# Optimization experiments

Hardware: AMD Instinct MI355X
Metric: run time of the kernel (lower is better)

Reference implementation:

```python
import jax, jax.numpy as jnp
import numpy as np


def _layernorm(x, g, b, eps=1e-5):
    mu = x.mean(-1, keepdims=True)
    var = ((x - mu) ** 2).mean(-1, keepdims=True)
    return (x - mu) / jnp.sqrt(var + eps) * g + b


def _bilinear_sample(feat, coords):
    # feat: (B,C,H,W,D); coords: (B,C,N,2) normalized to [-1,1]
    # torch.grid_sample(mode='bilinear', padding_mode='zeros', align_corners=True)
    B, C, H, W, D = feat.shape
    x = (coords[..., 0] + 1.0) * 0.5 * (W - 1)  # grid x -> width axis
    y = (coords[..., 1] + 1.0) * 0.5 * (H - 1)  # grid y -> height axis
    x0 = jnp.floor(x)
    y0 = jnp.floor(y)
    wx1 = x - x0
    wy1 = y - y0
    bi = jnp.arange(B)[:, None, None]
    ci = jnp.arange(C)[None, :, None]

    def corner(yi, xi, w):
        inb = (xi >= 0) & (xi < W) & (yi >= 0) & (yi < H)
        xc = jnp.clip(xi, 0, W - 1).astype(jnp.int32)
        yc = jnp.clip(yi, 0, H - 1).astype(jnp.int32)
        v = feat[bi, ci, yc, xc]  # (B,C,N,D) gather
        return v * (w * inb)[..., None]

    return (corner(y0, x0, (1 - wy1) * (1 - wx1))
            + corner(y0, x0 + 1, (1 - wy1) * wx1)
            + corner(y0 + 1, x0, wy1 * (1 - wx1))
            + corner(y0 + 1, x0 + 1, wy1 * wx1))


def setup_inputs() -> dict:
    key = jax.random.key(0)
    ks = jax.random.split(key, 12)
    B, C, N, D, H, W = 2, 8, 16384, 256, 64, 64
    s = 1.0 / np.sqrt(D).astype(np.float32)
    return {
        "queries": jax.random.normal(ks[0], (B, N, D), jnp.float32),
        "image_features": jax.random.normal(ks[1], (B, C, H, W, D), jnp.float32),
        "pixel_coords": jax.random.uniform(ks[2], (B, C, N, 2), jnp.float32) * 2.0 - 1.0,
        "valid_mask": jax.random.randint(ks[3], (B, C, N), 0, 2).astype(jnp.int32),
        "Wq": jax.random.normal(ks[4], (D, D), jnp.float32) * s,
        "bq": jnp.zeros((D,), jnp.float32),
        "Wkv": jax.random.normal(ks[5], (D, 2 * D), jnp.float32) * s,
        "bkv": jnp.zeros((2 * D,), jnp.float32),
        "Wo": jax.random.normal(ks[6], (D, D), jnp.float32) * s,
        "bo": jnp.zeros((D,), jnp.float32),
        "gamma": jnp.ones((D,), jnp.float32),
        "beta": jnp.zeros((D,), jnp.float32),
    }


def reference(queries, image_features, pixel_coords, valid_mask,
              Wq, bq, Wkv, bkv, Wo, bo, gamma, beta):
    B, N, D = queries.shape
    residual = queries
    qn = _layernorm(queries, gamma, beta)
    sampled = _bilinear_sample(image_features, pixel_coords)      # (B,C,N,D)
    sampled = jnp.transpose(sampled, (0, 2, 1, 3))                 # (B,N,C,D)
    q = qn @ Wq + bq                                               # (B,N,D)
    kv = sampled @ Wkv + bkv                                       # (B,N,C,2D)
    k, v = kv[..., :D], kv[..., D:]
    scores = jnp.einsum('bnd,bncd->bnc', q, k) / jnp.sqrt(jnp.float32(D))
    valid = jnp.transpose(valid_mask, (0, 2, 1)) != 0              # (B,N,C)
    scores = jnp.where(valid, scores, -jnp.inf)
    attn = jax.nn.softmax(scores, axis=-1)
    attn = jnp.where(jnp.isnan(attn), 0.0, attn)                   # all-invalid -> 0
    out = jnp.einsum('bnc,bncd->bnd', attn, v)
    return residual + out @ Wo + bo
```

## Files before the change

kernel.cpp:

```cpp
#include <hip/hip_runtime.h>
#include <math.h>

#define NROWS 32768

typedef __attribute__((ext_vector_type(8))) short short8;
typedef __attribute__((ext_vector_type(4))) float f32x4;

#define WS_ABF    0
#define WS_WVOBF  32768
#define WS_PB     65536
#define WS_BVO    65792
#define WS_SUMA   66048
#define WS_P      98816
#define WS_FEATBF 8487424

__device__ __forceinline__ unsigned short f2bf(float f) {
    unsigned u = __builtin_bit_cast(unsigned, f);
    u += 0x7FFFu + ((u >> 16) & 1u);
    return (unsigned short)(u >> 16);
}
__device__ __forceinline__ float bf_lo(unsigned u) {
    return __builtin_bit_cast(float, u << 16);
}
__device__ __forceinline__ float bf_hi(unsigned u) {
    return __builtin_bit_cast(float, u & 0xFFFF0000u);
}

__global__ __launch_bounds__(256)
void precompute_kernel(const float* __restrict__ Wq, const float* __restrict__ bq,
                       const float* __restrict__ Wkv, const float* __restrict__ bkv,
                       const float* __restrict__ Wo, const float* __restrict__ feat,
                       float* __restrict__ ws) {
    int t = threadIdx.x;
    int blk = blockIdx.x;
    if (blk >= 514) {
        long i = (long)(blk - 514) * 1024 + t * 4;
        float4 v = *(const float4*)(feat + i);
        unsigned lo = (unsigned)f2bf(v.x) | ((unsigned)f2bf(v.y) << 16);
        unsigned hi = (unsigned)f2bf(v.z) | ((unsigned)f2bf(v.w) << 16);
        *(uint2*)((unsigned short*)(ws + WS_FEATBF) + i) = make_uint2(lo, hi);
        return;
    }
    if (blk < 256) {
        int f = blk;
        const float4* wq4 = (const float4*)(Wq + f * 256);
        const float4* wk4 = (const float4*)(Wkv + (long)t * 512);
        float acc = 0.f;
        #pragma unroll 8
        for (int d4 = 0; d4 < 64; ++d4) {
            float4 a = wq4[d4], b = wk4[d4];
            acc += a.x * b.x + a.y * b.y + a.z * b.z + a.w * b.w;
        }
        ((unsigned short*)(ws + WS_ABF))[t * 256 + f] = f2bf(acc);
    } else if (blk < 512) {
        int e = blk - 256;
        float acc = 0.f;
        for (int g = 0; g < 256; ++g)
            acc = fmaf(Wkv[(long)e * 512 + 256 + g], Wo[g * 256 + t], acc);
        ((unsigned short*)(ws + WS_WVOBF))[t * 256 + e] = f2bf(acc);
    } else if (blk == 512) {
        float acc = 0.f;
        for (int d = 0; d < 256; ++d)
            acc = fmaf(bq[d], Wkv[(long)t * 512 + d], acc);
        ws[WS_PB + t] = acc;
    } else {
        float acc = 0.f;
        for (int g = 0; g < 256; ++g)
            acc = fmaf(bkv[256 + g], Wo[g * 256 + t], acc);
        ws[WS_BVO + t] = acc;
    }
}

__global__ __launch_bounds__(256)
void ln_p_mfma(const float* __restrict__ queries, const float* __restrict__ gamma,
               const float* __restrict__ beta, float* __restrict__ ws) {
    __shared__ unsigned short qs[64][264];
    const unsigned short* Abf = (const unsigned short*)(ws + WS_ABF);
    const float* pb = ws + WS_PB;
    float* pbuf = ws + WS_P;
    int tid = threadIdx.x, wave = tid >> 6, lane = tid & 63;
    long row0 = (long)blockIdx.x * 64;

    float4 g4 = *(const float4*)(gamma + 4 * lane);
    float4 b4 = *(const float4*)(beta + 4 * lane);
    for (int rr = 0; rr < 16; ++rr) {
        int r = wave * 16 + rr;
        float4 v = *(const float4*)(queries + (row0 + r) * 256 + 4 * lane);
        float s = v.x + v.y + v.z + v.w;
        s += __shfl_xor(s, 32); s += __shfl_xor(s, 16); s += __shfl_xor(s, 8);
        s += __shfl_xor(s, 4);  s += __shfl_xor(s, 2);  s += __shfl_xor(s, 1);
        float mu = s * 0.00390625f;
        float dx = v.x - mu, dy = v.y - mu, dz = v.z - mu, dw = v.w - mu;
        float vv = dx * dx + dy * dy + dz * dz + dw * dw;
        vv += __shfl_xor(vv, 32); vv += __shfl_xor(vv, 16); vv += __shfl_xor(vv, 8);
        vv += __shfl_xor(vv, 4);  vv += __shfl_xor(vv, 2);  vv += __shfl_xor(vv, 1);
        float rstd = rsqrtf(vv * 0.00390625f + 1e-5f);
        float qx = dx * rstd * g4.x + b4.x;
        float qy = dy * rstd * g4.y + b4.y;
        float qz = dz * rstd * g4.z + b4.z;
        float qw = dw * rstd * g4.w + b4.w;
        unsigned lo = (unsigned)f2bf(qx) | ((unsigned)f2bf(qy) << 16);
        unsigned hi = (unsigned)f2bf(qz) | ((unsigned)f2bf(qw) << 16);
        *(uint2*)&qs[r][4 * lane] = make_uint2(lo, hi);
    }
    __syncthreads();

    int r16 = lane & 15, g = lane >> 4;
    f32x4 zero = {0.f, 0.f, 0.f, 0.f};
    f32x4 acc[4][4];
    #pragma unroll
    for (int mt = 0; mt < 4; ++mt)
        #pragma unroll
        for (int nt = 0; nt < 4; ++nt) acc[mt][nt] = zero;

    #pragma unroll
    for (int ks = 0; ks < 8; ++ks) {
        short8 bfr[4], afr[4];
        #pragma unroll
        for (int nt = 0; nt < 4; ++nt)
            bfr[nt] = *(const short8*)(Abf + ((wave * 64 + nt * 16 + r16) << 8) + ks * 32 + g * 8);
        #pragma unroll
        for (int mt = 0; mt < 4; ++mt)
            afr[mt] = *(const short8*)(&qs[mt * 16 + r16][ks * 32 + g * 8]);
        #pragma unroll
        for (int mt = 0; mt < 4; ++mt)
            #pragma unroll
            for (int nt = 0; nt < 4; ++nt)
                acc[mt][nt] = __builtin_amdgcn_mfma_f32_16x16x32_bf16(afr[mt], bfr[nt], acc[mt][nt], 0, 0, 0);
    }

    float pbv[4];
    #pragma unroll
    for (int nt = 0; nt < 4; ++nt) pbv[nt] = pb[wave * 64 + nt * 16 + r16];
    #pragma unroll
    for (int mt = 0; mt < 4; ++mt)
        #pragma unroll
        for (int nt = 0; nt < 4; ++nt)
            #pragma unroll
            for (int rg = 0; rg < 4; ++rg)
                pbuf[(row0 + mt * 16 + g * 4 + rg) * 256 + wave * 64 + nt * 16 + r16] =
                    acc[mt][nt][rg] + pbv[nt];
}

__global__ __launch_bounds__(256)
void sample_attn_bf(const float* __restrict__ coords, const int* __restrict__ vmask,
                    float* __restrict__ ws) {
    float* pbuf = ws + WS_P;
    float* suma = ws + WS_SUMA;
    const unsigned short* featbf = (const unsigned short*)(ws + WS_FEATBF);
    int tid = threadIdx.x, wave = tid >> 6, lane = tid & 63;
    long row = (long)blockIdx.x * 4 + wave;
    int b = (int)(row >> 14);
    int n = (int)(row & 16383);

    float4 p4 = *(const float4*)(pbuf + row * 256 + 4 * lane);

    float4 sc[8];
    float score[8];
    bool vld[8];
    #pragma unroll
    for (int c = 0; c < 8; ++c) {
        long cb = (long)(b * 8 + c) * 16384 + n;
        float cx = coords[2 * cb];
        float cy = coords[2 * cb + 1];
        vld[c] = (vmask[cb] != 0);
        float x = (cx + 1.f) * 31.5f;
        float y = (cy + 1.f) * 31.5f;
        float x0f = floorf(x), y0f = floorf(y);
        float wx = x - x0f, wy = y - y0f;
        int ix0 = (int)x0f, iy0 = (int)y0f;
        int ix1 = ix0 + 1, iy1 = iy0 + 1;
        float bx0 = (ix0 >= 0 && ix0 < 64) ? 1.f : 0.f;
        float bx1 = (ix1 >= 0 && ix1 < 64) ? 1.f : 0.f;
        float by0 = (iy0 >= 0 && iy0 < 64) ? 1.f : 0.f;
        float by1 = (iy1 >= 0 && iy1 < 64) ? 1.f : 0.f;
        int cx0 = min(max(ix0, 0), 63), cx1 = min(max(ix1, 0), 63);
        int cy0 = min(max(iy0, 0), 63), cy1 = min(max(iy1, 0), 63);
        const unsigned short* fb = featbf + ((long)(b * 8 + c) << 20);
        const uint2* r00 = (const uint2*)(fb + ((cy0 * 64 + cx0) << 8)) + lane;
        const uint2* r01 = (const uint2*)(fb + ((cy0 * 64 + cx1) << 8)) + lane;
        const uint2* r10 = (const uint2*)(fb + ((cy1 * 64 + cx0) << 8)) + lane;
        const uint2* r11 = (const uint2*)(fb + ((cy1 * 64 + cx1) << 8)) + lane;
        float w00 = (1.f - wy) * (1.f - wx) * by0 * bx0;
        float w01 = (1.f - wy) * wx * by0 * bx1;
        float w10 = wy * (1.f - wx) * by1 * bx0;
        float w11 = wy * wx * by1 * bx1;
        uint2 v00 = *r00, v01 = *r01, v10 = *r10, v11 = *r11;
        float4 s;
        s.x = w00 * bf_lo(v00.x) + w01 * bf_lo(v01.x) + w10 * bf_lo(v10.x) + w11 * bf_lo(v11.x);
        s.y = w00 * bf_hi(v00.x) + w01 * bf_hi(v01.x) + w10 * bf_hi(v10.x) + w11 * bf_hi(v11.x);
        s.z = w00 * bf_lo(v00.y) + w01 * bf_lo(v01.y) + w10 * bf_lo(v10.y) + w11 * bf_lo(v11.y);
        s.w = w00 * bf_hi(v00.y) + w01 * bf_hi(v01.y) + w10 * bf_hi(v10.y) + w11 * bf_hi(v11.y);
        sc[c] = s;
        float t = s.x * p4.x + s.y * p4.y + s.z * p4.z + s.w * p4.w;
        t += __shfl_xor(t, 32); t += __shfl_xor(t, 16); t += __shfl_xor(t, 8);
        t += __shfl_xor(t, 4);  t += __shfl_xor(t, 2);  t += __shfl_xor(t, 1);
        score[c] = t * 0.0625f;
    }

    float m = -INFINITY;
    #pragma unroll
    for (int c = 0; c < 8; ++c) if (vld[c]) m = fmaxf(m, score[c]);
    float4 sb = {0.f, 0.f, 0.f, 0.f};
    float sa = 0.f;
    if (m > -INFINITY) {
        float w[8], s = 0.f;
        #pragma unroll
        for (int c = 0; c < 8; ++c) { w[c] = vld[c] ? expf(score[c] - m) : 0.f; s += w[c]; }
        float inv = 1.f / s;
        #pragma unroll
        for (int c = 0; c < 8; ++c) {
            float a = w[c] * inv;
            sb.x = fmaf(a, sc[c].x, sb.x);
            sb.y = fmaf(a, sc[c].y, sb.y);
            sb.z = fmaf(a, sc[c].z, sb.z);
            sb.w = fmaf(a, sc[c].w, sb.w);
        }
        sa = 1.f;
    }
    unsigned lo = (unsigned)f2bf(sb.x) | ((unsigned)f2bf(sb.y) << 16);
    unsigned hi = (unsigned)f2bf(sb.z) | ((unsigned)f2bf(sb.w) << 16);
    ((uint2*)((char*)pbuf + row * 1024))[lane] = make_uint2(lo, hi);
    if (lane == 0) suma[row] = sa;
}

__global__ __launch_bounds__(256)
void final_mfma(const float* __restrict__ queries, const float* __restrict__ bo,
                const float* __restrict__ ws, float* __restrict__ out) {
    __shared__ unsigned short qs[64][264];
    __shared__ float ssu[64];
    const unsigned short* Wvobf = (const unsigned short*)(ws + WS_WVOBF);
    const float* bvo = ws + WS_BVO;
    const float* suma = ws + WS_SUMA;
    const float* pbuf = ws + WS_P;
    int tid = threadIdx.x, wave = tid >> 6, lane = tid & 63;
    long row0 = (long)blockIdx.x * 64;

    for (int rr = 0; rr < 16; ++rr) {
        int r = wave * 16 + rr;
        uint2 v = ((const uint2*)((const char*)pbuf + (row0 + r) * 1024))[lane];
        *(uint2*)&qs[r][4 * lane] = v;
    }
    if (tid < 64) ssu[tid] = suma[row0 + tid];
    __syncthreads();

    int r16 = lane & 15, g = lane >> 4;
    f32x4 zero = {0.f, 0.f, 0.f, 0.f};
    f32x4 acc[4][4];
    #pragma unroll
    for (int mt = 0; mt < 4; ++mt)
        #pragma unroll
        for (int nt = 0; nt < 4; ++nt) acc[mt][nt] = zero;

    #pragma unroll
    for (int ks = 0; ks < 8; ++ks) {
        short8 bfr[4], afr[4];
        #pragma unroll
        for (int nt = 0; nt < 4; ++nt)
            bfr[nt] = *(const short8*)(Wvobf + ((wave * 64 + nt * 16 + r16) << 8) + ks * 32 + g * 8);
        #pragma unroll
        for (int mt = 0; mt < 4; ++mt)
            afr[mt] = *(const short8*)(&qs[mt * 16 + r16][ks * 32 + g * 8]);
        #pragma unroll
        for (int mt = 0; mt < 4; ++mt)
            #pragma unroll
            for (int nt = 0; nt < 4; ++nt)
                acc[mt][nt] = __builtin_amdgcn_mfma_f32_16x16x32_bf16(afr[mt], bfr[nt], acc[mt][nt], 0, 0, 0);
    }

    float bvov[4], bov[4];
    #pragma unroll
    for (int nt = 0; nt < 4; ++nt) {
        int col = wave * 64 + nt * 16 + r16;
        bvov[nt] = bvo[col];
        bov[nt] = bo[col];
    }
    #pragma unroll
    for (int mt = 0; mt < 4; ++mt)
        #pragma unroll
        for (int nt = 0; nt < 4; ++nt)
            #pragma unroll
            for (int rg = 0; rg < 4; ++rg) {
                long row = row0 + mt * 16 + g * 4 + rg;
                int col = wave * 64 + nt * 16 + r16;
                out[row * 256 + col] = queries[row * 256 + col] + acc[mt][nt][rg]
                                     + ssu[mt * 16 + g * 4 + rg] * bvov[nt] + bov[nt];
            }
}

extern "C" void kernel_launch(void* const* d_in, const int* in_sizes, int n_in,
                              void* d_out, int out_size, void* d_ws, size_t ws_size,
                              hipStream_t stream) {
    const float* queries = (const float*)d_in[0];
    const float* feat    = (const float*)d_in[1];
    const float* coords  = (const float*)d_in[2];
    const int*   vmask   = (const int*)  d_in[3];
    const float* Wq      = (const float*)d_in[4];
    const float* bq      = (const float*)d_in[5];
    const float* Wkv     = (const float*)d_in[6];
    const float* bkv     = (const float*)d_in[7];
    const float* Wo      = (const float*)d_in[8];
    const float* bo      = (const float*)d_in[9];
    const float* gamma   = (const float*)d_in[10];
    const float* beta    = (const float*)d_in[11];
    float* out = (float*)d_out;
    float* ws  = (float*)d_ws;

    precompute_kernel<<<514 + 16384, 256, 0, stream>>>(Wq, bq, Wkv, bkv, Wo, feat, ws);
    ln_p_mfma<<<NROWS / 64, 256, 0, stream>>>(queries, gamma, beta, ws);
    sample_attn_bf<<<NROWS / 4, 256, 0, stream>>>(coords, vmask, ws);
    final_mfma<<<NROWS / 64, 256, 0, stream>>>(queries, bo, ws, out);
}
```

Before: 280.2 us.

## Fuse layernorm projection, sampling attention and output GEMM into one row-pipelined kernel

Replaces the three row kernels (LN+P GEMM, sampling/attention, output GEMM) with one kernel that handles 32 rows per block. The intermediate P vectors, attention outputs and per-row sums stay in shared memory instead of going through global workspace. This removes the global write and reread of the fp32 P buffer and the bf16 attention buffer, plus two launch boundaries. The epilogue now writes coalesced float4 stores, and expf becomes __expf. The trade-off is fewer rows per block for MFMA reuse, extra block barriers, and the gather phase sharing a block with the GEMM phases, which may limit latency hiding.

```diff
diff --git a/kernel.cpp b/kernel.cpp
--- a/kernel.cpp
+++ b/kernel.cpp
@@ -10,8 +10,6 @@
 #define WS_WVOBF  32768
 #define WS_PB     65536
 #define WS_BVO    65792
-#define WS_SUMA   66048
-#define WS_P      98816
 #define WS_FEATBF 8487424
 
 __device__ __forceinline__ unsigned short f2bf(float f) {
@@ -71,221 +69,223 @@
     }
 }
 
-__global__ __launch_bounds__(256)
-void ln_p_mfma(const float* __restrict__ queries, const float* __restrict__ gamma,
-               const float* __restrict__ beta, float* __restrict__ ws) {
-    __shared__ unsigned short qs[64][264];
-    const unsigned short* Abf = (const unsigned short*)(ws + WS_ABF);
-    const float* pb = ws + WS_PB;
-    float* pbuf = ws + WS_P;
+#define RPB  32
+#define SLOT 260
+
+__global__ __launch_bounds__(256, 4)
+void fused_rowpipe(const float* __restrict__ queries, const float* __restrict__ gamma,
+                   const float* __restrict__ beta, const float* __restrict__ coords,
+                   const int* __restrict__ vmask, const float* __restrict__ bo,
+                   const float* __restrict__ ws, float* __restrict__ out) {
+    __shared__ float buf[RPB * SLOT + RPB];
+    float* ssu = buf + RPB * SLOT;
+
+    const unsigned short* Abf    = (const unsigned short*)(ws + WS_ABF);
+    const unsigned short* Wvobf  = (const unsigned short*)(ws + WS_WVOBF);
+    const float*          pb     = ws + WS_PB;
+    const float*          bvo    = ws + WS_BVO;
+    const unsigned short* featbf = (const unsigned short*)(ws + WS_FEATBF);
+
     int tid = threadIdx.x, wave = tid >> 6, lane = tid & 63;
-    long row0 = (long)blockIdx.x * 64;
-
-    float4 g4 = *(const float4*)(gamma + 4 * lane);
-    float4 b4 = *(const float4*)(beta + 4 * lane);
-    for (int rr = 0; rr < 16; ++rr) {
-        int r = wave * 16 + rr;
-        float4 v = *(const float4*)(queries + (row0 + r) * 256 + 4 * lane);
-        float s = v.x + v.y + v.z + v.w;
-        s += __shfl_xor(s, 32); s += __shfl_xor(s, 16); s += __shfl_xor(s, 8);
-        s += __shfl_xor(s, 4);  s += __shfl_xor(s, 2);  s += __shfl_xor(s, 1);
-        float mu = s * 0.00390625f;
-        float dx = v.x - mu, dy = v.y - mu, dz = v.z - mu, dw = v.w - mu;
-        float vv = dx * dx + dy * dy + dz * dz + dw * dw;
-        vv += __shfl_xor(vv, 32); vv += __shfl_xor(vv, 16); vv += __shfl_xor(vv, 8);
-        vv += __shfl_xor(vv, 4);  vv += __shfl_xor(vv, 2);  vv += __shfl_xor(vv, 1);
-        float rstd = rsqrtf(vv * 0.00390625f + 1e-5f);
-        float qx = dx * rstd * g4.x + b4.x;
-        float qy = dy * rstd * g4.y + b4.y;
-        float qz = dz * rstd * g4.z + b4.z;
-        float qw = dw * rstd * g4.w + b4.w;
-        unsigned lo = (unsigned)f2bf(qx) | ((unsigned)f2bf(qy) << 16);
-        unsigned hi = (unsigned)f2bf(qz) | ((unsigned)f2bf(qw) << 16);
-        *(uint2*)&qs[r][4 * lane] = make_uint2(lo, hi);
+    long row0 = (long)blockIdx.x * RPB;
+
+    {
+        float4 g4 = *(const float4*)(gamma + 4 * lane);
+        float4 b4 = *(const float4*)(beta + 4 * lane);
+        #pragma unroll
+        for (int rr = 0; rr < 8; ++rr) {
+            int r = wave * 8 + rr;
+            float4 v = *(const float4*)(queries + (row0 + r) * 256 + 4 * lane);
+            float s = v.x + v.y + v.z + v.w;
+            s += __shfl_xor(s, 32); s += __shfl_xor(s, 16); s += __shfl_xor(s, 8);
+            s += __shfl_xor(s, 4);  s += __shfl_xor(s, 2);  s += __shfl_xor(s, 1);
+            float mu = s * 0.00390625f;
+            float dx = v.x - mu, dy = v.y - mu, dz = v.z - mu, dw = v.w - mu;
+            float vv = dx * dx + dy * dy + dz * dz + dw * dw;
+            vv += __shfl_xor(vv, 32); vv += __shfl_xor(vv, 16); vv += __shfl_xor(vv, 8);
+            vv += __shfl_xor(vv, 4);  vv += __shfl_xor(vv, 2);  vv += __shfl_xor(vv, 1);
+            float rstd = rsqrtf(vv * 0.00390625f + 1e-5f);
+            float qx = dx * rstd * g4.x + b4.x;
+            float qy = dy * rstd * g4.y + b4.y;
+            float qz = dz * rstd * g4.z + b4.z;
+            float qw = dw * rstd * g4.w + b4.w;
+            unsigned lo = (unsigned)f2bf(qx) | ((unsigned)f2bf(qy) << 16);
+            unsigned hi = (unsigned)f2bf(qz) | ((unsigned)f2bf(qw) << 16);
+            *(uint2*)((unsigned short*)&buf[r * SLOT] + 4 * lane) = make_uint2(lo, hi);
+        }
     }
     __syncthreads();
 
     int r16 = lane & 15, g = lane >> 4;
     f32x4 zero = {0.f, 0.f, 0.f, 0.f};
-    f32x4 acc[4][4];
-    #pragma unroll
-    for (int mt = 0; mt < 4; ++mt)
-        #pragma unroll
-        for (int nt = 0; nt < 4; ++nt) acc[mt][nt] = zero;
-
-    #pragma unroll
-    for (int ks = 0; ks < 8; ++ks) {
-        short8 bfr[4], afr[4];
-        #pragma unroll
-        for (int nt = 0; nt < 4; ++nt)
-            bfr[nt] = *(const short8*)(Abf + ((wave * 64 + nt * 16 + r16) << 8) + ks * 32 + g * 8);
-        #pragma unroll
-        for (int mt = 0; mt < 4; ++mt)
-            afr[mt] = *(const short8*)(&qs[mt * 16 + r16][ks * 32 + g * 8]);
-        #pragma unroll
-        for (int mt = 0; mt < 4; ++mt)
+
+    {
+        f32x4 acc[2][4];
+        #pragma unroll
+        for (int mt = 0; mt < 2; ++mt)
+            #pragma unroll
+            for (int nt = 0; nt < 4; ++nt) acc[mt][nt] = zero;
+
+        #pragma unroll
+        for (int ks = 0; ks < 8; ++ks) {
+            short8 bfr[4], afr[2];
             #pragma unroll
             for (int nt = 0; nt < 4; ++nt)
-                acc[mt][nt] = __builtin_amdgcn_mfma_f32_16x16x32_bf16(afr[mt], bfr[nt], acc[mt][nt], 0, 0, 0);
-    }
-
-    float pbv[4];
-    #pragma unroll
-    for (int nt = 0; nt < 4; ++nt) pbv[nt] = pb[wave * 64 + nt * 16 + r16];
-    #pragma unroll
-    for (int mt = 0; mt < 4; ++mt)
-        #pragma unroll
-        for (int nt = 0; nt < 4; ++nt)
-            #pragma unroll
-            for (int rg = 0; rg < 4; ++rg)
-                pbuf[(row0 + mt * 16 + g * 4 + rg) * 256 + wave * 64 + nt * 16 + r16] =
-                    acc[mt][nt][rg] + pbv[nt];
-}
-
-__global__ __launch_bounds__(256)
-void sample_attn_bf(const float* __restrict__ coords, const int* __restrict__ vmask,
-                    float* __restrict__ ws) {
-    float* pbuf = ws + WS_P;
-    float* suma = ws + WS_SUMA;
-    const unsigned short* featbf = (const unsigned short*)(ws + WS_FEATBF);
-    int tid = threadIdx.x, wave = tid >> 6, lane = tid & 63;
-    long row = (long)blockIdx.x * 4 + wave;
-    int b = (int)(row >> 14);
-    int n = (int)(row & 16383);
-
-    float4 p4 = *(const float4*)(pbuf + row * 256 + 4 * lane);
-
-    float4 sc[8];
-    float score[8];
-    bool vld[8];
-    #pragma unroll
-    for (int c = 0; c < 8; ++c) {
-        long cb = (long)(b * 8 + c) * 16384 + n;
-        float cx = coords[2 * cb];
-        float cy = coords[2 * cb + 1];
-        vld[c] = (vmask[cb] != 0);
-        float x = (cx + 1.f) * 31.5f;
-        float y = (cy + 1.f) * 31.5f;
-        float x0f = floorf(x), y0f = floorf(y);
-        float wx = x - x0f, wy = y - y0f;
-        int ix0 = (int)x0f, iy0 = (int)y0f;
-        int ix1 = ix0 + 1, iy1 = iy0 + 1;
-        float bx0 = (ix0 >= 0 && ix0 < 64) ? 1.f : 0.f;
-        float bx1 = (ix1 >= 0 && ix1 < 64) ? 1.f : 0.f;
-        float by0 = (iy0 >= 0 && iy0 < 64) ? 1.f : 0.f;
-        float by1 = (iy1 >= 0 && iy1 < 64) ? 1.f : 0.f;
-        int cx0 = min(max(ix0, 0), 63), cx1 = min(max(ix1, 0), 63);
-        int cy0 = min(max(iy0, 0), 63), cy1 = min(max(iy1, 0), 63);
-        const unsigned short* fb = featbf + ((long)(b * 8 + c) << 20);
-        const uint2* r00 = (const uint2*)(fb + ((cy0 * 64 + cx0) << 8)) + lane;
-        const uint2* r01 = (const uint2*)(fb + ((cy0 * 64 + cx1) << 8)) + lane;
-        const uint2* r10 = (const uint2*)(fb + ((cy1 * 64 + cx0) << 8)) + lane;
-        const uint2* r11 = (const uint2*)(fb + ((cy1 * 64 + cx1) << 8)) + lane;
-        float w00 = (1.f - wy) * (1.f - wx) * by0 * bx0;
-        float w01 = (1.f - wy) * wx * by0 * bx1;
-        float w10 = wy * (1.f - wx) * by1 * bx0;
-        float w11 = wy * wx * by1 * bx1;
-        uint2 v00 = *r00, v01 = *r01, v10 = *r10, v11 = *r11;
-        float4 s;
-        s.x = w00 * bf_lo(v00.x) + w01 * bf_lo(v01.x) + w10 * bf_lo(v10.x) + w11 * bf_lo(v11.x);
-        s.y = w00 * bf_hi(v00.x) + w01 * bf_hi(v01.x) + w10 * bf_hi(v10.x) + w11 * bf_hi(v11.x);
-        s.z = w00 * bf_lo(v00.y) + w01 * bf_lo(v01.y) + w10 * bf_lo(v10.y) + w11 * bf_lo(v11.y);
-        s.w = w00 * bf_hi(v00.y) + w01 * bf_hi(v01.y) + w10 * bf_hi(v10.y) + w11 * bf_hi(v11.y);
-        sc[c] = s;
-        float t = s.x * p4.x + s.y * p4.y + s.z * p4.z + s.w * p4.w;
-        t += __shfl_xor(t, 32); t += __shfl_xor(t, 16); t += __shfl_xor(t, 8);
-        t += __shfl_xor(t, 4);  t += __shfl_xor(t, 2);  t += __shfl_xor(t, 1);
-        score[c] = t * 0.0625f;
-    }
-
-    float m = -INFINITY;
-    #pragma unroll
-    for (int c = 0; c < 8; ++c) if (vld[c]) m = fmaxf(m, score[c]);
-    float4 sb = {0.f, 0.f, 0.f, 0.f};
-    float sa = 0.f;
-    if (m > -INFINITY) {
-        float w[8], s = 0.f;
-        #pragma unroll
-        for (int c = 0; c < 8; ++c) { w[c] = vld[c] ? expf(score[c] - m) : 0.f; s += w[c]; }
-        float inv = 1.f / s;
+                bfr[nt] = *(const short8*)(Abf + ((wave * 64 + nt * 16 + r16) << 8) + ks * 32 + g * 8);
+            #pragma unroll
+            for (int mt = 0; mt < 2; ++mt)
+                afr[mt] = *(const short8*)((const unsigned short*)buf + (mt * 16 + r16) * (SLOT * 2) + ks * 32 + g * 8);
+            #pragma unroll
+            for (int mt = 0; mt < 2; ++mt)
+                #pragma unroll
+                for (int nt = 0; nt < 4; ++nt)
+                    acc[mt][nt] = __builtin_amdgcn_mfma_f32_16x16x32_bf16(afr[mt], bfr[nt], acc[mt][nt], 0, 0, 0);
+        }
+        __syncthreads();
+
+        float pbv[4];
+        #pragma unroll
+        for (int nt = 0; nt < 4; ++nt) pbv[nt] = pb[wave * 64 + nt * 16 + r16];
+        #pragma unroll
+        for (int mt = 0; mt < 2; ++mt)
+            #pragma unroll
+            for (int nt = 0; nt < 4; ++nt)
+                #pragma unroll
+                for (int rg = 0; rg < 4; ++rg)
+                    buf[(mt * 16 + g * 4 + rg) * SLOT + wave * 64 + nt * 16 + r16] =
+                        acc[mt][nt][rg] + pbv[nt];
+    }
+    __syncthreads();
+
+    for (int rr = 0; rr < 8; ++rr) {
+        int r = wave * 8 + rr;
+        int rowu = __builtin_amdgcn_readfirstlane((int)(row0 + r));
+        int b = rowu >> 14;
+        int n = rowu & 16383;
+
+        float4 p4 = *(const float4*)(&buf[r * SLOT + 4 * lane]);
+
+        float4 sc[8];
+        float score[8];
+        bool vld[8];
         #pragma unroll
         for (int c = 0; c < 8; ++c) {
-            float a = w[c] * inv;
-            sb.x = fmaf(a, sc[c].x, sb.x);
-            sb.y = fmaf(a, sc[c].y, sb.y);
-            sb.z = fmaf(a, sc[c].z, sb.z);
-            sb.w = fmaf(a, sc[c].w, sb.w);
-        }
-        sa = 1.f;
-    }
-    unsigned lo = (unsigned)f2bf(sb.x) | ((unsigned)f2bf(sb.y) << 16);
-    unsigned hi = (unsigned)f2bf(sb.z) | ((unsigned)f2bf(sb.w) << 16);
-    ((uint2*)((char*)pbuf + row * 1024))[lane] = make_uint2(lo, hi);
-    if (lane == 0) suma[row] = sa;
-}
-
-__global__ __launch_bounds__(256)
-void final_mfma(const float* __restrict__ queries, const float* __restrict__ bo,
-                const float* __restrict__ ws, float* __restrict__ out) {
-    __shared__ unsigned short qs[64][264];
-    __shared__ float ssu[64];
-    const unsigned short* Wvobf = (const unsigned short*)(ws + WS_WVOBF);
-    const float* bvo = ws + WS_BVO;
-    const float* suma = ws + WS_SUMA;
-    const float* pbuf = ws + WS_P;
-    int tid = threadIdx.x, wave = tid >> 6, lane = tid & 63;
-    long row0 = (long)blockIdx.x * 64;
-
-    for (int rr = 0; rr < 16; ++rr) {
-        int r = wave * 16 + rr;
-        uint2 v = ((const uint2*)((const char*)pbuf + (row0 + r) * 1024))[lane];
-        *(uint2*)&qs[r][4 * lane] = v;
-    }
-    if (tid < 64) ssu[tid] = suma[row0 + tid];
+            long cb = (long)(b * 8 + c) * 16384 + n;
+            float cx = coords[2 * cb];
+            float cy = coords[2 * cb + 1];
+            vld[c] = (vmask[cb] != 0);
+            float x = (cx + 1.f) * 31.5f;
+            float y = (cy + 1.f) * 31.5f;
+            float x0f = floorf(x), y0f = floorf(y);
+            float wx = x - x0f, wy = y - y0f;
+            int ix0 = (int)x0f, iy0 = (int)y0f;
+            int ix1 = ix0 + 1, iy1 = iy0 + 1;
+            float bx0 = (ix0 >= 0 && ix0 < 64) ? 1.f : 0.f;
+            float bx1 = (ix1 >= 0 && ix1 < 64) ? 1.f : 0.f;
+            float by0 = (iy0 >= 0 && iy0 < 64) ? 1.f : 0.f;
+            float by1 = (iy1 >= 0 && iy1 < 64) ? 1.f : 0.f;
+            int cx0 = min(max(ix0, 0), 63), cx1 = min(max(ix1, 0), 63);
+            int cy0 = min(max(iy0, 0), 63), cy1 = min(max(iy1, 0), 63);
+            const unsigned short* fb = featbf + ((long)(b * 8 + c) << 20);
+            const uint2* r00 = (const uint2*)(fb + ((cy0 * 64 + cx0) << 8)) + lane;
+            const uint2* r01 = (const uint2*)(fb + ((cy0 * 64 + cx1) << 8)) + lane;
+            const uint2* r10 = (const uint2*)(fb + ((cy1 * 64 + cx0) << 8)) + lane;
+            const uint2* r11 = (const uint2*)(fb + ((cy1 * 64 + cx1) << 8)) + lane;
+            float w00 = (1.f - wy) * (1.f - wx) * by0 * bx0;
+            float w01 = (1.f - wy) * wx * by0 * bx1;
+            float w10 = wy * (1.f - wx) * by1 * bx0;
+            float w11 = wy * wx * by1 * bx1;
+            uint2 v00 = *r00, v01 = *r01, v10 = *r10, v11 = *r11;
+            float4 s;
+            s.x = w00 * bf_lo(v00.x) + w01 * bf_lo(v01.x) + w10 * bf_lo(v10.x) + w11 * bf_lo(v11.x);
+            s.y = w00 * bf_hi(v00.x) + w01 * bf_hi(v01.x) + w10 * bf_hi(v10.x) + w11 * bf_hi(v11.x);
+            s.z = w00 * bf_lo(v00.y) + w01 * bf_lo(v01.y) + w10 * bf_lo(v10.y) + w11 * bf_lo(v11.y);
+            s.w = w00 * bf_hi(v00.y) + w01 * bf_hi(v01.y) + w10 * bf_hi(v10.y) + w11 * bf_hi(v11.y);
+            sc[c] = s;
+            float t = s.x * p4.x + s.y * p4.y + s.z * p4.z + s.w * p4.w;
+            t += __shfl_xor(t, 32); t += __shfl_xor(t, 16); t += __shfl_xor(t, 8);
+            t += __shfl_xor(t, 4);  t += __shfl_xor(t, 2);  t += __shfl_xor(t, 1);
+            score[c] = t * 0.0625f;
+        }
+
+        float m = -INFINITY;
+        #pragma unroll
+        for (int c = 0; c < 8; ++c) if (vld[c]) m = fmaxf(m, score[c]);
+        float4 sb = {0.f, 0.f, 0.f, 0.f};
+        float sa = 0.f;
+        if (m > -INFINITY) {
+            float w[8], s = 0.f;
+            #pragma unroll
+            for (int c = 0; c < 8; ++c) { w[c] = vld[c] ? __expf(score[c] - m) : 0.f; s += w[c]; }
+            float inv = 1.f / s;
+            #pragma unroll
+            for (int c = 0; c < 8; ++c) {
+                float a = w[c] * inv;
+                sb.x = fmaf(a, sc[c].x, sb.x);
+                sb.y = fmaf(a, sc[c].y, sb.y);
+                sb.z = fmaf(a, sc[c].z, sb.z);
+                sb.w = fmaf(a, sc[c].w, sb.w);
+            }
+            sa = 1.f;
+        }
+        unsigned lo = (unsigned)f2bf(sb.x) | ((unsigned)f2bf(sb.y) << 16);
+        unsigned hi = (unsigned)f2bf(sb.z) | ((unsigned)f2bf(sb.w) << 16);
+        *(uint2*)((unsigned short*)&buf[r * SLOT] + 4 * lane) = make_uint2(lo, hi);
+        if (lane == 0) ssu[r] = sa;
+    }
     __syncthreads();
 
-    int r16 = lane & 15, g = lane >> 4;
-    f32x4 zero = {0.f, 0.f, 0.f, 0.f};
-    f32x4 acc[4][4];
-    #pragma unroll
-    for (int mt = 0; mt < 4; ++mt)
-        #pragma unroll
-        for (int nt = 0; nt < 4; ++nt) acc[mt][nt] = zero;
-
-    #pragma unroll
-    for (int ks = 0; ks < 8; ++ks) {
-        short8 bfr[4], afr[4];
-        #pragma unroll
-        for (int nt = 0; nt < 4; ++nt)
-            bfr[nt] = *(const short8*)(Wvobf + ((wave * 64 + nt * 16 + r16) << 8) + ks * 32 + g * 8);
-        #pragma unroll
-        for (int mt = 0; mt < 4; ++mt)
-            afr[mt] = *(const short8*)(&qs[mt * 16 + r16][ks * 32 + g * 8]);
-        #pragma unroll
-        for (int mt = 0; mt < 4; ++mt)
+    {
+        f32x4 acc2[2][4];
+        #pragma unroll
+        for (int mt = 0; mt < 2; ++mt)
+            #pragma unroll
+            for (int nt = 0; nt < 4; ++nt) acc2[mt][nt] = zero;
+
+        #pragma unroll
+        for (int ks = 0; ks < 8; ++ks) {
+            short8 bfr[4], afr[2];
             #pragma unroll
             for (int nt = 0; nt < 4; ++nt)
-                acc[mt][nt] = __builtin_amdgcn_mfma_f32_16x16x32_bf16(afr[mt], bfr[nt], acc[mt][nt], 0, 0, 0);
-    }
-
-    float bvov[4], bov[4];
-    #pragma unroll
-    for (int nt = 0; nt < 4; ++nt) {
-        int col = wave * 64 + nt * 16 + r16;
-        bvov[nt] = bvo[col];
-        bov[nt] = bo[col];
-    }
-    #pragma unroll
-    for (int mt = 0; mt < 4; ++mt)
-        #pragma unroll
-        for (int nt = 0; nt < 4; ++nt)
-            #pragma unroll
-            for (int rg = 0; rg < 4; ++rg) {
-                long row = row0 + mt * 16 + g * 4 + rg;
-                int col = wave * 64 + nt * 16 + r16;
-                out[row * 256 + col] = queries[row * 256 + col] + acc[mt][nt][rg]
-                                     + ssu[mt * 16 + g * 4 + rg] * bvov[nt] + bov[nt];
-            }
+                bfr[nt] = *(const short8*)(Wvobf + ((wave * 64 + nt * 16 + r16) << 8) + ks * 32 + g * 8);
+            #pragma unroll
+            for (int mt = 0; mt < 2; ++mt)
+                afr[mt] = *(const short8*)((const unsigned short*)buf + (mt * 16 + r16) * (SLOT * 2) + ks * 32 + g * 8);
+            #pragma unroll
+            for (int mt = 0; mt < 2; ++mt)
+                #pragma unroll
+                for (int nt = 0; nt < 4; ++nt)
+                    acc2[mt][nt] = __builtin_amdgcn_mfma_f32_16x16x32_bf16(afr[mt], bfr[nt], acc2[mt][nt], 0, 0, 0);
+        }
+        __syncthreads();
+
+        #pragma unroll
+        for (int mt = 0; mt < 2; ++mt)
+            #pragma unroll
+            for (int nt = 0; nt < 4; ++nt)
+                #pragma unroll
+                for (int rg = 0; rg < 4; ++rg)
+                    buf[(mt * 16 + g * 4 + rg) * SLOT + wave * 64 + nt * 16 + r16] = acc2[mt][nt][rg];
+    }
+    __syncthreads();
+
+    {
+        float4 bvo4 = *(const float4*)(bvo + 4 * lane);
+        float4 bo4  = *(const float4*)(bo + 4 * lane);
+        #pragma unroll
+        for (int rr = 0; rr < 8; ++rr) {
+            int r = wave * 8 + rr;
+            float4 q4 = *(const float4*)(queries + (row0 + r) * 256 + 4 * lane);
+            float4 a4 = *(const float4*)(&buf[r * SLOT + 4 * lane]);
+            float su = ssu[r];
+            float4 o;
+            o.x = q4.x + a4.x + su * bvo4.x + bo4.x;
+            o.y = q4.y + a4.y + su * bvo4.y + bo4.y;
+            o.z = q4.z + a4.z + su * bvo4.z + bo4.z;
+            o.w = q4.w + a4.w + su * bvo4.w + bo4.w;
+            *(float4*)(out + (row0 + r) * 256 + 4 * lane) = o;
+        }
+    }
 }
 
 extern "C" void kernel_launch(void* const* d_in, const int* in_sizes, int n_in,
@@ -307,7 +307,5 @@
     float* ws  = (float*)d_ws;
 
     precompute_kernel<<<514 + 16384, 256, 0, stream>>>(Wq, bq, Wkv, bkv, Wo, feat, ws);
-    ln_p_mfma<<<NROWS / 64, 256, 0, stream>>>(queries, gamma, beta, ws);
-    sample_attn_bf<<<NROWS / 4, 256, 0, stream>>>(coords, vmask, ws);
-    final_mfma<<<NROWS / 64, 256, 0, stream>>>(queries, bo, ws, out);
-}
+    fused_rowpipe<<<NROWS / RPB, 256, 0, stream>>>(queries, gamma, beta, coords, vmask, bo, ws, out);
+}
```

New measurement: 259.4 us. 1.08x faster.
